# Kernel optimization log

Measured on AMD Instinct MI355X. Metric: run time of the kernel, lower is better.

## Reference

```python
import jax, jax.numpy as jnp
import numpy as np

FEA, DK, H = 512, 64, 8
B, L = 4, 2048
EPS = 1e-5


def _layernorm(x, g, b):
    mu = jnp.mean(x, axis=-1, keepdims=True)
    var = jnp.mean(jnp.square(x - mu), axis=-1, keepdims=True)
    return (x - mu) * jax.lax.rsqrt(var + EPS) * g + b


def setup_inputs() -> dict:
    key = jax.random.key(0)
    ks = jax.random.split(key, 12)
    d = {
        'qx': jax.random.normal(ks[0], (B, L, FEA), jnp.float32),
        'kx': jax.random.normal(ks[1], (B, L, FEA), jnp.float32),
        'vx': jax.random.normal(ks[2], (B, L, FEA), jnp.float32),
        'maskPAD': jax.random.randint(ks[3], (B, L, L), 0, 2, jnp.int32),
        # attention projections (stored as [in, out]); biases zero-init as in module
        'wq': jax.random.normal(ks[4], (FEA, DK * H), jnp.float32) * 0.02,
        'bq': jnp.zeros((DK * H,), jnp.float32),
        'wk': jax.random.normal(ks[5], (FEA, DK * H), jnp.float32) * 0.02,
        'bk': jnp.zeros((DK * H,), jnp.float32),
        'wv': jax.random.normal(ks[6], (FEA, DK * H), jnp.float32) * 0.02,
        'bv': jnp.zeros((DK * H,), jnp.float32),
        'wo': jax.random.normal(ks[7], (DK * H, FEA), jnp.float32) * 0.02,
        'bo': jnp.zeros((FEA,), jnp.float32),
        # FFN
        'w1': jax.random.normal(ks[8], (FEA, 4 * FEA), jnp.float32) * 0.02,
        'b1': jnp.zeros((4 * FEA,), jnp.float32),
        'w2': jax.random.normal(ks[9], (4 * FEA, FEA), jnp.float32) * 0.02,
        'b2': jnp.zeros((FEA,), jnp.float32),
        # layer norms
        'ln1_g': jnp.ones((FEA,), jnp.float32),
        'ln1_b': jnp.zeros((FEA,), jnp.float32),
        'ln2_g': jnp.ones((FEA,), jnp.float32),
        'ln2_b': jnp.zeros((FEA,), jnp.float32),
    }
    return d


def reference(qx, kx, vx, maskPAD, wq, bq, wk, bk, wv, bv, wo, bo,
              w1, b1, w2, b2, ln1_g, ln1_b, ln2_g, ln2_b):
    b, l, _ = qx.shape
    # project and split heads: [B, H, L, DK]
    q = (qx @ wq + bq).reshape(b, l, H, DK).transpose(0, 2, 1, 3)
    k = (kx @ wk + bk).reshape(b, l, H, DK).transpose(0, 2, 1, 3)
    v = (vx @ wv + bv).reshape(b, l, H, DK).transpose(0, 2, 1, 3)
    scores = jnp.einsum('bhqd,bhkd->bhqk', q, k) / np.sqrt(DK)  # [B,H,L,L]
    mask = (maskPAD == 0)[:, None, :, :]
    scores = jnp.where(mask, jnp.float32(-2 ** 15 + 1), scores)
    alpha = jax.nn.softmax(scores, axis=-1)
    z = jnp.einsum('bhqk,bhkd->bhqd', alpha, v)  # [B,H,L,DK]
    z = z.transpose(0, 2, 1, 3).reshape(b, l, H * DK)
    z = z @ wo + bo
    # post-LN FFN block (dropout = identity at inference)
    zn = _layernorm(vx + z, ln1_g, ln1_b)
    ffn = jax.nn.gelu(zn @ w1 + b1, approximate=False) @ w2 + b2
    return _layernorm(zn + ffn, ln2_g, ln2_b)
```

## Files before the change

kernel.cpp:

```cpp
#include <hip/hip_runtime.h>
#include <cstdint>


typedef __bf16 bf16;
typedef __bf16 bf16x4 __attribute__((ext_vector_type(4)));
typedef __bf16 bf16x8 __attribute__((ext_vector_type(8)));
typedef float floatx4 __attribute__((ext_vector_type(4)));

__device__ __forceinline__ floatx4 mfma_bf16(bf16x8 a, bf16x8 b, floatx4 c) {
  return __builtin_amdgcn_mfma_f32_16x16x32_bf16(a, b, c, 0, 0, 0);
}

__device__ __forceinline__ void load_lds_16(const void* g, void* l) {
  auto gp = reinterpret_cast<const void __attribute__((address_space(1)))*>(
      reinterpret_cast<uintptr_t>(g));
  auto lp = reinterpret_cast<void __attribute__((address_space(3)))*>(
      (unsigned int)reinterpret_cast<uintptr_t>(l));
  __builtin_amdgcn_global_load_lds(gp, lp, 16, 0, 0);
}

__device__ __forceinline__ float gelu_f(float x) {
  float t = 0.7978845608f * (x + 0.044715f * x * x * x);
  float e = __builtin_amdgcn_exp2f(t * 2.885390082f);
  float th = 1.0f - 2.0f * __builtin_amdgcn_rcpf(e + 1.0f);
  return 0.5f * x * (1.0f + th);
}

#define PLANE128 2064
#define PLANE64 1040
#define PSTR 72

__global__ void __launch_bounds__(256) transpose4_k(const float* __restrict__ w0,
                                                    const float* __restrict__ w1,
                                                    const float* __restrict__ w2,
                                                    const float* __restrict__ w3,
                                                    bf16* __restrict__ o0,
                                                    bf16* __restrict__ o1,
                                                    bf16* __restrict__ o2,
                                                    bf16* __restrict__ o3) {
  const float* in = (blockIdx.z == 0) ? w0 : (blockIdx.z == 1) ? w1
                    : (blockIdx.z == 2) ? w2 : w3;
  bf16* out = (blockIdx.z == 0) ? o0 : (blockIdx.z == 1) ? o1
              : (blockIdx.z == 2) ? o2 : o3;
  __shared__ float tile[32][33];
  int m0 = blockIdx.x * 32, k0 = blockIdx.y * 32;
  int tx = threadIdx.x, ty = threadIdx.y;
  for (int i = ty; i < 32; i += 8)
    tile[i][tx] = in[(size_t)(k0 + i) * 512 + m0 + tx];
  __syncthreads();
  for (int i = ty; i < 32; i += 8)
    out[(size_t)(m0 + i) * 512 + k0 + tx] = (bf16)tile[tx][i];
}

__global__ void __launch_bounds__(256) transpose_k(const float* __restrict__ in,
                                                   bf16* __restrict__ out,
                                                   int K, int M) {
  __shared__ float tile[32][33];
  int m0 = blockIdx.x * 32, k0 = blockIdx.y * 32;
  int tx = threadIdx.x, ty = threadIdx.y;
  for (int i = ty; i < 32; i += 8)
    tile[i][tx] = in[(size_t)(k0 + i) * M + m0 + tx];
  __syncthreads();
  for (int i = ty; i < 32; i += 8)
    out[(size_t)(m0 + i) * K + k0 + tx] = (bf16)tile[tx][i];
}

__global__ void __launch_bounds__(256) cvt3_k(const float* __restrict__ a,
                                              const float* __restrict__ b,
                                              const float* __restrict__ c,
                                              bf16* __restrict__ out) {
  int seg = blockIdx.x >> 12;
  const float* in = (seg == 0) ? a : (seg == 1) ? b : c;
  int i = ((blockIdx.x & 4095) * 256 + threadIdx.x) * 4;
  float4 v = *(const float4*)(in + i);
  bf16x4 o;
  o[0] = (bf16)v.x; o[1] = (bf16)v.y; o[2] = (bf16)v.z; o[3] = (bf16)v.w;
  *(bf16x4*)(out + (size_t)seg * 4194304 + i) = o;
}

__global__ void __launch_bounds__(256) maskbits_k(const int* __restrict__ m,
                                                  unsigned long long* __restrict__ out) {
  int w = blockIdx.x * 4 + (threadIdx.x >> 6);
  int lane = threadIdx.x & 63;
  int v = m[(size_t)w * 64 + lane];
  unsigned long long b = __ballot(v != 0);
  if (lane == 0) out[w] = b;
}

template <int EPI>
__device__ __forceinline__ void epi_store(void* Cout, int n, int m, int M,
                                          float val) {
  if constexpr (EPI == 1) {
    int bb = n >> 11, l = n & 2047, hh = m >> 6, d = m & 63;
    ((bf16*)Cout)[((size_t)((bb * 8 + hh) * 2048 + l)) * 64 + d] = (bf16)val;
  } else if constexpr (EPI == 2) {
    int bb = n >> 11, l = n & 2047, hh = m >> 6, d = m & 63;
    ((bf16*)Cout)[((size_t)((bb * 8 + hh) * 64 + d)) * 2048 + l] = (bf16)val;
  } else if constexpr (EPI == 3) {
    ((bf16*)Cout)[(size_t)n * M + m] = (bf16)gelu_f(val);
  } else if constexpr (EPI == 4) {
    ((float*)Cout)[(size_t)n * M + m] = val;
  } else {
    ((float*)Cout)[(size_t)n * M + m] += val;
  }
}

template <int EPI, bool TALL>
__global__ void __launch_bounds__(256) gemm_bt(const bf16* __restrict__ A,
                                               const bf16* __restrict__ Bt,
                                               const float* __restrict__ bias,
                                               void* __restrict__ Cout,
                                               int M, int K, int lda, int ldb) {
  __shared__ __attribute__((aligned(16))) char As[8 * PLANE128];
  __shared__ __attribute__((aligned(16))) char Bs[TALL ? 8 * PLANE64 : 8 * PLANE128];
  int tid = threadIdx.x, wave = tid >> 6, lane = tid & 63;
  int lrow = lane & 15, quad = lane >> 4;
  int n0 = blockIdx.y * 128;
  int m0 = blockIdx.x * (TALL ? 64 : 128);
  int wr = wave >> 1, wc = wave & 1;
  floatx4 zero4 = {0.f, 0.f, 0.f, 0.f};
  constexpr int NI = TALL ? 2 : 4;
  floatx4 acc[NI][4];
#pragma unroll
  for (int i = 0; i < NI; ++i)
#pragma unroll
    for (int j = 0; j < 4; ++j) acc[i][j] = zero4;
  for (int k0 = 0; k0 < K; k0 += 64) {
    __syncthreads();
#pragma unroll
    for (int h = 0; h < 2; ++h) {
      int p = wave + 4 * h;
#pragma unroll
      for (int j = 0; j < 2; ++j) {
        int row = j * 64 + lane;
        load_lds_16(A + (size_t)(n0 + row) * lda + k0 + p * 8,
                    As + p * PLANE128 + j * 1024 + lane * 16);
      }
      if constexpr (TALL) {
        load_lds_16(Bt + (size_t)(m0 + lane) * ldb + k0 + p * 8,
                    Bs + p * PLANE64 + lane * 16);
      } else {
#pragma unroll
        for (int j = 0; j < 2; ++j) {
          int row = j * 64 + lane;
          load_lds_16(Bt + (size_t)(m0 + row) * ldb + k0 + p * 8,
                      Bs + p * PLANE128 + j * 1024 + lane * 16);
        }
      }
    }
    __syncthreads();
#pragma unroll
    for (int h = 0; h < 2; ++h) {
      int pb = h * 4 + quad;
      bf16x8 af[NI], bfr[4];
#pragma unroll
      for (int i = 0; i < NI; ++i) {
        int row = (TALL ? wave * 32 : wr * 64) + i * 16 + lrow;
        af[i] = *(const bf16x8*)(As + pb * PLANE128 + row * 16);
      }
#pragma unroll
      for (int j = 0; j < 4; ++j) {
        if constexpr (TALL)
          bfr[j] = *(const bf16x8*)(Bs + pb * PLANE64 + (j * 16 + lrow) * 16);
        else
          bfr[j] = *(const bf16x8*)(Bs + pb * PLANE128 +
                                    (wc * 64 + j * 16 + lrow) * 16);
      }
#pragma unroll
      for (int i = 0; i < NI; ++i)
#pragma unroll
        for (int j = 0; j < 4; ++j)
          acc[i][j] = mfma_bf16(af[i], bfr[j], acc[i][j]);
    }
  }
  float bv[4];
#pragma unroll
  for (int j = 0; j < 4; ++j) {
    int m = m0 + (TALL ? 0 : wc * 64) + j * 16 + lrow;
    bv[j] = (EPI == 5) ? 0.f : bias[m];
  }
#pragma unroll
  for (int i = 0; i < NI; ++i)
#pragma unroll
    for (int j = 0; j < 4; ++j)
#pragma unroll
      for (int r = 0; r < 4; ++r) {
        int n = n0 + (TALL ? wave * 32 : wr * 64) + i * 16 + quad * 4 + r;
        int m = m0 + (TALL ? 0 : wc * 64) + j * 16 + lrow;
        epi_store<EPI>(Cout, n, m, M, acc[i][j][r] + bv[j]);
      }
}

__global__ void __launch_bounds__(256) qkv2_k(const bf16* __restrict__ xall,
                                              const bf16* __restrict__ wqT,
                                              const bf16* __restrict__ wkT,
                                              const bf16* __restrict__ wvT,
                                              const float* __restrict__ bq,
                                              const float* __restrict__ bk,
                                              const float* __restrict__ bv_,
                                              bf16* __restrict__ qh,
                                              bf16* __restrict__ kh,
                                              bf16* __restrict__ vt) {
  __shared__ __attribute__((aligned(16))) char As[8 * PLANE128];
  __shared__ __attribute__((aligned(16))) char Bs[8 * PLANE128];
  int tid = threadIdx.x, wave = tid >> 6, lane = tid & 63;
  int lrow = lane & 15, quad = lane >> 4;
  int seg = blockIdx.y >> 6;
  int n0 = (blockIdx.y & 63) * 128, m0 = blockIdx.x * 128;
  const bf16* A = xall + (size_t)seg * 4194304;
  const bf16* Bt = (seg == 0) ? wqT : (seg == 1) ? wkT : wvT;
  const float* bias = (seg == 0) ? bq : (seg == 1) ? bk : bv_;
  bf16* out = (seg == 0) ? qh : (seg == 1) ? kh : vt;
  int wr = wave >> 1, wc = wave & 1;
  floatx4 zero4 = {0.f, 0.f, 0.f, 0.f};
  floatx4 acc[4][4];
#pragma unroll
  for (int i = 0; i < 4; ++i)
#pragma unroll
    for (int j = 0; j < 4; ++j) acc[i][j] = zero4;
  for (int k0 = 0; k0 < 512; k0 += 64) {
    __syncthreads();
#pragma unroll
    for (int h = 0; h < 2; ++h) {
      int p = wave + 4 * h;
#pragma unroll
      for (int j = 0; j < 2; ++j) {
        int row = j * 64 + lane;
        load_lds_16(A + (size_t)(n0 + row) * 512 + k0 + p * 8,
                    As + p * PLANE128 + j * 1024 + lane * 16);
        load_lds_16(Bt + (size_t)(m0 + row) * 512 + k0 + p * 8,
                    Bs + p * PLANE128 + j * 1024 + lane * 16);
      }
    }
    __syncthreads();
#pragma unroll
    for (int h = 0; h < 2; ++h) {
      int pb = h * 4 + quad;
      bf16x8 af[4], bfr[4];
#pragma unroll
      for (int t = 0; t < 4; ++t) {
        af[t] = *(const bf16x8*)(As + pb * PLANE128 + (wr * 64 + t * 16 + lrow) * 16);
        bfr[t] = *(const bf16x8*)(Bs + pb * PLANE128 + (wc * 64 + t * 16 + lrow) * 16);
      }
#pragma unroll
      for (int i = 0; i < 4; ++i)
#pragma unroll
        for (int j = 0; j < 4; ++j) acc[i][j] = mfma_bf16(af[i], bfr[j], acc[i][j]);
    }
  }
  float bvv[4];
#pragma unroll
  for (int j = 0; j < 4; ++j) bvv[j] = bias[m0 + wc * 64 + j * 16 + lrow];
#pragma unroll
  for (int i = 0; i < 4; ++i)
#pragma unroll
    for (int j = 0; j < 4; ++j)
#pragma unroll
      for (int r = 0; r < 4; ++r) {
        int n = n0 + wr * 64 + i * 16 + quad * 4 + r;
        int m = m0 + wc * 64 + j * 16 + lrow;
        float val = acc[i][j][r] + bvv[j];
        int bb = n >> 11, l = n & 2047, hh = m >> 6, d = m & 63;
        if (seg == 2)
          out[((size_t)((bb * 8 + hh) * 64 + d)) * 2048 + l] = (bf16)val;
        else
          out[((size_t)((bb * 8 + hh) * 2048 + l)) * 64 + d] = (bf16)val;
      }
}

__global__ void __launch_bounds__(256) qkv_k(const float* __restrict__ qx,
                                             const float* __restrict__ kx,
                                             const float* __restrict__ vx,
                                             const bf16* __restrict__ wqT,
                                             const bf16* __restrict__ wkT,
                                             const bf16* __restrict__ wvT,
                                             const float* __restrict__ bq,
                                             const float* __restrict__ bk,
                                             const float* __restrict__ bv_,
                                             bf16* __restrict__ qh,
                                             bf16* __restrict__ kh,
                                             bf16* __restrict__ vt) {
  __shared__ __attribute__((aligned(16))) char As[8 * PLANE128];
  __shared__ __attribute__((aligned(16))) char Bs[8 * PLANE128];
  int tid = threadIdx.x, wave = tid >> 6, lane = tid & 63;
  int lrow = lane & 15, quad = lane >> 4;
  int seg = blockIdx.y >> 6;
  int n0 = (blockIdx.y & 63) * 128, m0 = blockIdx.x * 128;
  const float* Af = (seg == 0) ? qx : (seg == 1) ? kx : vx;
  const bf16* Bt = (seg == 0) ? wqT : (seg == 1) ? wkT : wvT;
  const float* bias = (seg == 0) ? bq : (seg == 1) ? bk : bv_;
  bf16* out = (seg == 0) ? qh : (seg == 1) ? kh : vt;
  int wr = wave >> 1, wc = wave & 1;
  floatx4 zero4 = {0.f, 0.f, 0.f, 0.f};
  floatx4 acc[4][4];
#pragma unroll
  for (int i = 0; i < 4; ++i)
#pragma unroll
    for (int j = 0; j < 4; ++j) acc[i][j] = zero4;
  int arow = tid >> 2, ap = tid & 3;
  for (int k0 = 0; k0 < 512; k0 += 64) {
    bf16x8 a[4];
#pragma unroll
    for (int u = 0; u < 4; ++u) {
      int row = arow + (u & 1) * 64, p = ap + (u >> 1) * 4;
      const float* src = Af + (size_t)(n0 + row) * 512 + k0 + p * 8;
      float4 x0 = *(const float4*)src;
      float4 x1 = *(const float4*)(src + 4);
      a[u][0] = (bf16)x0.x; a[u][1] = (bf16)x0.y; a[u][2] = (bf16)x0.z;
      a[u][3] = (bf16)x0.w; a[u][4] = (bf16)x1.x; a[u][5] = (bf16)x1.y;
      a[u][6] = (bf16)x1.z; a[u][7] = (bf16)x1.w;
    }
    __syncthreads();
#pragma unroll
    for (int u = 0; u < 4; ++u) {
      int row = arow + (u & 1) * 64, p = ap + (u >> 1) * 4;
      *(bf16x8*)(As + p * PLANE128 + row * 16) = a[u];
    }
#pragma unroll
    for (int h = 0; h < 2; ++h) {
      int p = wave + 4 * h;
#pragma unroll
      for (int j = 0; j < 2; ++j) {
        int row = j * 64 + lane;
        load_lds_16(Bt + (size_t)(m0 + row) * 512 + k0 + p * 8,
                    Bs + p * PLANE128 + j * 1024 + lane * 16);
      }
    }
    __syncthreads();
#pragma unroll
    for (int h = 0; h < 2; ++h) {
      int pb = h * 4 + quad;
      bf16x8 af[4], bfr[4];
#pragma unroll
      for (int t = 0; t < 4; ++t) {
        af[t] = *(const bf16x8*)(As + pb * PLANE128 + (wr * 64 + t * 16 + lrow) * 16);
        bfr[t] = *(const bf16x8*)(Bs + pb * PLANE128 + (wc * 64 + t * 16 + lrow) * 16);
      }
#pragma unroll
      for (int i = 0; i < 4; ++i)
#pragma unroll
        for (int j = 0; j < 4; ++j) acc[i][j] = mfma_bf16(af[i], bfr[j], acc[i][j]);
    }
  }
  float bvv[4];
#pragma unroll
  for (int j = 0; j < 4; ++j) bvv[j] = bias[m0 + wc * 64 + j * 16 + lrow];
#pragma unroll
  for (int i = 0; i < 4; ++i)
#pragma unroll
    for (int j = 0; j < 4; ++j)
#pragma unroll
      for (int r = 0; r < 4; ++r) {
        int n = n0 + wr * 64 + i * 16 + quad * 4 + r;
        int m = m0 + wc * 64 + j * 16 + lrow;
        float val = acc[i][j][r] + bvv[j];
        int bb = n >> 11, l = n & 2047, hh = m >> 6, d = m & 63;
        if (seg == 2)
          out[((size_t)((bb * 8 + hh) * 64 + d)) * 2048 + l] = (bf16)val;
        else
          out[((size_t)((bb * 8 + hh) * 2048 + l)) * 64 + d] = (bf16)val;
      }
}

__global__ void __launch_bounds__(256) attn_k(const bf16* __restrict__ Qh,
                                              const bf16* __restrict__ Kh,
                                              const bf16* __restrict__ Vt,
                                              const unsigned long long* __restrict__ MB,
                                              bf16* __restrict__ Z) {
  __shared__ __attribute__((aligned(16))) char Ks[8 * PLANE64];
  __shared__ __attribute__((aligned(16))) char Vs[8 * PLANE64];
  __shared__ __attribute__((aligned(16))) bf16 Pt[4][16 * PSTR];
  int qt = blockIdx.x, h = blockIdx.y, b = blockIdx.z;
  int tid = threadIdx.x, wave = tid >> 6, lane = tid & 63;
  int lrow = lane & 15, quad = lane >> 4;
  int q0 = qt * 64;
  size_t headbase = (size_t)(b * 8 + h) * 2048 * 64;

  const bf16* Qp = Qh + headbase + (size_t)(q0 + wave * 16 + lrow) * 64 + quad * 8;
  bf16x8 qf0 = *(const bf16x8*)Qp;
  bf16x8 qf1 = *(const bf16x8*)(Qp + 32);

  floatx4 zero4 = {0.f, 0.f, 0.f, 0.f};
  floatx4 o_acc[4], acc_l = zero4;
#pragma unroll
  for (int dt = 0; dt < 4; ++dt) o_acc[dt] = zero4;
  bf16x8 ones;
#pragma unroll
  for (int j = 0; j < 8; ++j) ones[j] = (bf16)1.0f;

  const bf16* Vg = Vt + headbase;
  const unsigned long long* MBrow =
      MB + ((size_t)b * 2048 + q0 + wave * 16 + lrow) * 32;
  bf16* Pw = Pt[wave];
  const float C = 0.1803368801f;

  for (int kt = 0; kt < 32; ++kt) {
    int kk0 = kt * 64;
    const bf16* Kg = Kh + headbase + (size_t)kk0 * 64;
    __syncthreads();
#pragma unroll
    for (int j = 0; j < 2; ++j) {
      int p = wave * 2 + j;
      load_lds_16(Kg + (size_t)lane * 64 + p * 8, Ks + p * PLANE64 + lane * 16);
      load_lds_16(Vg + (size_t)lane * 2048 + kk0 + p * 8,
                  Vs + p * PLANE64 + lane * 16);
    }
    unsigned long long mw = MBrow[kt];
    unsigned sx = (unsigned)(mw >> (quad * 4));
    unsigned sy = (unsigned)(mw >> (32 + quad * 4));
    __syncthreads();

#pragma unroll
    for (int nt = 0; nt < 4; ++nt) {
      int R = nt * 16 + lrow;
      bf16x8 k0f = *(const bf16x8*)(Ks + quad * PLANE64 + R * 16);
      bf16x8 k1f = *(const bf16x8*)(Ks + (quad + 4) * PLANE64 + R * 16);
      floatx4 aa = zero4;
      aa = mfma_bf16(k0f, qf0, aa);
      aa = mfma_bf16(k1f, qf1, aa);
      unsigned sel = (nt < 2 ? sx : sy) >> ((nt & 1) * 16);
      bf16x4 pv;
#pragma unroll
      for (int r = 0; r < 4; ++r) {
        float e = __builtin_amdgcn_exp2f(aa[r] * C);
        pv[r] = (bf16)(((sel >> r) & 1u) ? e : 0.f);
      }
      *(bf16x4*)(Pw + lrow * PSTR + nt * 16 + quad * 4) = pv;
    }
    bf16x8 pf0 = *(const bf16x8*)(Pw + lrow * PSTR + quad * 8);
    bf16x8 pf1 = *(const bf16x8*)(Pw + lrow * PSTR + 32 + quad * 8);
    acc_l = mfma_bf16(ones, pf0, acc_l);
    acc_l = mfma_bf16(ones, pf1, acc_l);
#pragma unroll
    for (int dt = 0; dt < 4; ++dt) {
      int R = dt * 16 + lrow;
      bf16x8 v0 = *(const bf16x8*)(Vs + quad * PLANE64 + R * 16);
      bf16x8 v1 = *(const bf16x8*)(Vs + (quad + 4) * PLANE64 + R * 16);
      o_acc[dt] = mfma_bf16(v0, pf0, o_acc[dt]);
      o_acc[dt] = mfma_bf16(v1, pf1, o_acc[dt]);
    }
  }
  float lr = __builtin_amdgcn_rcpf(acc_l[0]);
  size_t zrow = ((size_t)(b * 2048 + q0 + wave * 16 + lrow)) * 512 + h * 64;
#pragma unroll
  for (int dt = 0; dt < 4; ++dt) {
    bf16x4 ov;
#pragma unroll
    for (int r = 0; r < 4; ++r) ov[r] = (bf16)(o_acc[dt][r] * lr);
    *(bf16x4*)(Z + zrow + dt * 16 + quad * 4) = ov;
  }
}

template <bool A_BF16, bool OUT_BF16>
__global__ void __launch_bounds__(256) ln_k(const void* __restrict__ a_,
                                            const float* __restrict__ s,
                                            const float* __restrict__ g,
                                            const float* __restrict__ bta,
                                            void* __restrict__ out_) {
  int row = blockIdx.x * 4 + (threadIdx.x >> 6);
  int lane = threadIdx.x & 63;
  size_t base = (size_t)row * 512 + lane * 8;
  float x[8];
  float4 sa = *(const float4*)(s + base);
  float4 sb = *(const float4*)(s + base + 4);
  if constexpr (A_BF16) {
    bf16x8 av = *(const bf16x8*)((const bf16*)a_ + base);
    x[0] = (float)av[0] + sa.x; x[1] = (float)av[1] + sa.y;
    x[2] = (float)av[2] + sa.z; x[3] = (float)av[3] + sa.w;
    x[4] = (float)av[4] + sb.x; x[5] = (float)av[5] + sb.y;
    x[6] = (float)av[6] + sb.z; x[7] = (float)av[7] + sb.w;
  } else {
    float4 a0 = *(const float4*)((const float*)a_ + base);
    float4 a1 = *(const float4*)((const float*)a_ + base + 4);
    x[0] = a0.x + sa.x; x[1] = a0.y + sa.y; x[2] = a0.z + sa.z; x[3] = a0.w + sa.w;
    x[4] = a1.x + sb.x; x[5] = a1.y + sb.y; x[6] = a1.z + sb.z; x[7] = a1.w + sb.w;
  }
  float sum = 0.f;
#pragma unroll
  for (int i = 0; i < 8; ++i) sum += x[i];
#pragma unroll
  for (int off = 1; off < 64; off <<= 1) sum += __shfl_xor(sum, off, 64);
  float mu = sum * (1.0f / 512.0f);
  float vs = 0.f;
#pragma unroll
  for (int i = 0; i < 8; ++i) { float d = x[i] - mu; vs += d * d; }
#pragma unroll
  for (int off = 1; off < 64; off <<= 1) vs += __shfl_xor(vs, off, 64);
  float rstd = rsqrtf(vs * (1.0f / 512.0f) + 1e-5f);
  float4 g0 = *(const float4*)(g + lane * 8);
  float4 g1 = *(const float4*)(g + lane * 8 + 4);
  float4 b0 = *(const float4*)(bta + lane * 8);
  float4 b1 = *(const float4*)(bta + lane * 8 + 4);
  float gg[8] = {g0.x, g0.y, g0.z, g0.w, g1.x, g1.y, g1.z, g1.w};
  float bb[8] = {b0.x, b0.y, b0.z, b0.w, b1.x, b1.y, b1.z, b1.w};
  if constexpr (OUT_BF16) {
    bf16x8 o;
#pragma unroll
    for (int i = 0; i < 8; ++i)
      o[i] = (bf16)((x[i] - mu) * rstd * gg[i] + bb[i]);
    *(bf16x8*)((bf16*)out_ + base) = o;
  } else {
    float4 o0, o1;
    o0.x = (x[0] - mu) * rstd * gg[0] + bb[0];
    o0.y = (x[1] - mu) * rstd * gg[1] + bb[1];
    o0.z = (x[2] - mu) * rstd * gg[2] + bb[2];
    o0.w = (x[3] - mu) * rstd * gg[3] + bb[3];
    o1.x = (x[4] - mu) * rstd * gg[4] + bb[4];
    o1.y = (x[5] - mu) * rstd * gg[5] + bb[5];
    o1.z = (x[6] - mu) * rstd * gg[6] + bb[6];
    o1.w = (x[7] - mu) * rstd * gg[7] + bb[7];
    *(float4*)((float*)out_ + base) = o0;
    *(float4*)((float*)out_ + base + 4) = o1;
  }
}

extern "C" void kernel_launch(void* const* d_in, const int* in_sizes, int n_in,
                              void* d_out, int out_size, void* d_ws, size_t ws_size,
                              hipStream_t stream) {
  const float* qx = (const float*)d_in[0];
  const float* kx = (const float*)d_in[1];
  const float* vx = (const float*)d_in[2];
  const int* maskPAD = (const int*)d_in[3];
  const float* wq = (const float*)d_in[4];
  const float* bq = (const float*)d_in[5];
  const float* wk = (const float*)d_in[6];
  const float* bk = (const float*)d_in[7];
  const float* wv = (const float*)d_in[8];
  const float* bv = (const float*)d_in[9];
  const float* wo = (const float*)d_in[10];
  const float* bo = (const float*)d_in[11];
  const float* w1 = (const float*)d_in[12];
  const float* b1 = (const float*)d_in[13];
  const float* w2 = (const float*)d_in[14];
  const float* b2 = (const float*)d_in[15];
  const float* g1 = (const float*)d_in[16];
  const float* be1 = (const float*)d_in[17];
  const float* g2 = (const float*)d_in[18];
  const float* be2 = (const float*)d_in[19];

  char* w = (char*)d_ws;
  size_t off = 0;
  auto alloc = [&](size_t bytes) {
    void* p = w + off;
    off += (bytes + 255) & ~(size_t)255;
    return p;
  };
  bf16* wqT = (bf16*)alloc(512 * 512 * 2);
  bf16* wkT = (bf16*)alloc(512 * 512 * 2);
  bf16* wvT = (bf16*)alloc(512 * 512 * 2);
  bf16* woT = (bf16*)alloc(512 * 512 * 2);
  bf16* w1T = (bf16*)alloc(2048 * 512 * 2);
  bf16* w2T = (bf16*)alloc(512 * 2048 * 2);
  unsigned long long* mbits = (unsigned long long*)alloc((size_t)4 * 2048 * 32 * 8);
  size_t xall_bytes = (size_t)3 * 8192 * 512 * 2;
  size_t act4 = (size_t)8192 * 512 * 2;
  bool fast = (off + xall_bytes + 4 * (act4 + 256)) <= ws_size;
  bf16* xall = fast ? (bf16*)alloc(xall_bytes) : nullptr;
  bf16* qh = (bf16*)alloc(act4);
  bf16* kh = (bf16*)alloc(act4);
  bf16* vt = (bf16*)alloc(act4);
  bf16* z = (bf16*)alloc(act4);
  float* s12;
  bf16* zn;
  if (fast) {
    s12 = (float*)xall;
    zn = (bf16*)((char*)xall + (size_t)8192 * 512 * 4);
  } else {
    s12 = (float*)qh;
    zn = vt;
  }
  size_t h1_bytes = (size_t)8192 * 2048 * 2;
  bool big = (off + h1_bytes) <= ws_size;
  bf16* h1 = big ? (bf16*)alloc(h1_bytes) : z;

  dim3 tb(32, 8);
  transpose4_k<<<dim3(16, 16, 4), tb, 0, stream>>>(wq, wk, wv, wo, wqT, wkT, wvT, woT);
  transpose_k<<<dim3(64, 16), tb, 0, stream>>>(w1, w1T, 512, 2048);
  transpose_k<<<dim3(16, 64), tb, 0, stream>>>(w2, w2T, 2048, 512);
  maskbits_k<<<65536, 256, 0, stream>>>(maskPAD, mbits);
  if (fast) {
    cvt3_k<<<12288, 256, 0, stream>>>(qx, kx, vx, xall);
    qkv2_k<<<dim3(4, 192), 256, 0, stream>>>(xall, wqT, wkT, wvT, bq, bk, bv,
                                             qh, kh, vt);
  } else {
    qkv_k<<<dim3(4, 192), 256, 0, stream>>>(qx, kx, vx, wqT, wkT, wvT, bq, bk,
                                            bv, qh, kh, vt);
  }
  attn_k<<<dim3(32, 8, 4), 256, 0, stream>>>(qh, kh, vt, mbits, z);
  gemm_bt<4, true><<<dim3(8, 64), 256, 0, stream>>>(z, woT, bo, s12, 512, 512,
                                                    512, 512);
  ln_k<false, true><<<2048, 256, 0, stream>>>(vx, s12, g1, be1, zn);
  if (big) {
    gemm_bt<3, false><<<dim3(16, 64), 256, 0, stream>>>(zn, w1T, b1, h1, 2048,
                                                        512, 512, 512);
    gemm_bt<4, true><<<dim3(8, 64), 256, 0, stream>>>(h1, w2T, b2, s12, 512,
                                                      2048, 2048, 2048);
  } else {
    for (int p = 0; p < 4; ++p) {
      gemm_bt<3, true><<<dim3(8, 64), 256, 0, stream>>>(
          zn, w1T + (size_t)p * 512 * 512, b1 + p * 512, h1, 512, 512, 512, 512);
      if (p == 0)
        gemm_bt<4, true><<<dim3(8, 64), 256, 0, stream>>>(
            h1, w2T + p * 512, b2, s12, 512, 512, 512, 2048);
      else
        gemm_bt<5, true><<<dim3(8, 64), 256, 0, stream>>>(
            h1, w2T + p * 512, nullptr, s12, 512, 512, 512, 2048);
    }
  }
  ln_k<true, false><<<2048, 256, 0, stream>>>(zn, s12, g2, be2, (float*)d_out);
}
```

Baseline: 469.1 us.

## Double-buffer LDS tiles in GEMM, QKV and attention kernels to overlap loads

```diff
diff --git a/kernel.cpp b/kernel.cpp
--- a/kernel.cpp
+++ b/kernel.cpp
@@ -90,13 +90,7 @@
 template <int EPI>
 __device__ __forceinline__ void epi_store(void* Cout, int n, int m, int M,
                                           float val) {
-  if constexpr (EPI == 1) {
-    int bb = n >> 11, l = n & 2047, hh = m >> 6, d = m & 63;
-    ((bf16*)Cout)[((size_t)((bb * 8 + hh) * 2048 + l)) * 64 + d] = (bf16)val;
-  } else if constexpr (EPI == 2) {
-    int bb = n >> 11, l = n & 2047, hh = m >> 6, d = m & 63;
-    ((bf16*)Cout)[((size_t)((bb * 8 + hh) * 64 + d)) * 2048 + l] = (bf16)val;
-  } else if constexpr (EPI == 3) {
+  if constexpr (EPI == 3) {
     ((bf16*)Cout)[(size_t)n * M + m] = (bf16)gelu_f(val);
   } else if constexpr (EPI == 4) {
     ((float*)Cout)[(size_t)n * M + m] = val;
@@ -111,8 +105,11 @@
                                                const float* __restrict__ bias,
                                                void* __restrict__ Cout,
                                                int M, int K, int lda, int ldb) {
-  __shared__ __attribute__((aligned(16))) char As[8 * PLANE128];
-  __shared__ __attribute__((aligned(16))) char Bs[TALL ? 8 * PLANE64 : 8 * PLANE128];
+  constexpr int BK = TALL ? 64 : 32;
+  constexpr int NPL = BK / 8;
+  constexpr int BSZ = TALL ? NPL * PLANE64 : NPL * PLANE128;
+  __shared__ __attribute__((aligned(16))) char As[2][NPL * PLANE128];
+  __shared__ __attribute__((aligned(16))) char Bs[2][BSZ];
   int tid = threadIdx.x, wave = tid >> 6, lane = tid & 63;
   int lrow = lane & 15, quad = lane >> 4;
   int n0 = blockIdx.y * 128;
@@ -125,49 +122,68 @@
   for (int i = 0; i < NI; ++i)
 #pragma unroll
     for (int j = 0; j < 4; ++j) acc[i][j] = zero4;
-  for (int k0 = 0; k0 < K; k0 += 64) {
-    __syncthreads();
-#pragma unroll
-    for (int h = 0; h < 2; ++h) {
-      int p = wave + 4 * h;
+
+  auto stage = [&](int buf, int k0) {
+    if constexpr (TALL) {
+#pragma unroll
+      for (int h = 0; h < 2; ++h) {
+        int p = wave + 4 * h;
+#pragma unroll
+        for (int j = 0; j < 2; ++j) {
+          int row = j * 64 + lane;
+          load_lds_16(A + (size_t)(n0 + row) * lda + k0 + p * 8,
+                      As[buf] + p * PLANE128 + j * 1024 + lane * 16);
+        }
+        load_lds_16(Bt + (size_t)(m0 + lane) * ldb + k0 + p * 8,
+                    Bs[buf] + p * PLANE64 + lane * 16);
+      }
+    } else {
 #pragma unroll
       for (int j = 0; j < 2; ++j) {
         int row = j * 64 + lane;
-        load_lds_16(A + (size_t)(n0 + row) * lda + k0 + p * 8,
-                    As + p * PLANE128 + j * 1024 + lane * 16);
-      }
-      if constexpr (TALL) {
-        load_lds_16(Bt + (size_t)(m0 + lane) * ldb + k0 + p * 8,
-                    Bs + p * PLANE64 + lane * 16);
-      } else {
-#pragma unroll
-        for (int j = 0; j < 2; ++j) {
-          int row = j * 64 + lane;
-          load_lds_16(Bt + (size_t)(m0 + row) * ldb + k0 + p * 8,
-                      Bs + p * PLANE128 + j * 1024 + lane * 16);
-        }
-      }
-    }
+        load_lds_16(A + (size_t)(n0 + row) * lda + k0 + wave * 8,
+                    As[buf] + wave * PLANE128 + j * 1024 + lane * 16);
+        load_lds_16(Bt + (size_t)(m0 + row) * ldb + k0 + wave * 8,
+                    Bs[buf] + wave * PLANE128 + j * 1024 + lane * 16);
+      }
+    }
+  };
+
+  stage(0, 0);
+  int nit = K / BK;
+  for (int it = 0; it < nit; ++it) {
+    int cur = it & 1;
     __syncthreads();
-#pragma unroll
-    for (int h = 0; h < 2; ++h) {
-      int pb = h * 4 + quad;
-      bf16x8 af[NI], bfr[4];
-#pragma unroll
-      for (int i = 0; i < NI; ++i) {
-        int row = (TALL ? wave * 32 : wr * 64) + i * 16 + lrow;
-        af[i] = *(const bf16x8*)(As + pb * PLANE128 + row * 16);
-      }
-#pragma unroll
-      for (int j = 0; j < 4; ++j) {
-        if constexpr (TALL)
-          bfr[j] = *(const bf16x8*)(Bs + pb * PLANE64 + (j * 16 + lrow) * 16);
-        else
-          bfr[j] = *(const bf16x8*)(Bs + pb * PLANE128 +
-                                    (wc * 64 + j * 16 + lrow) * 16);
-      }
-#pragma unroll
-      for (int i = 0; i < NI; ++i)
+    if (it + 1 < nit) stage(cur ^ 1, (it + 1) * BK);
+    if constexpr (TALL) {
+#pragma unroll
+      for (int h = 0; h < 2; ++h) {
+        int pb = h * 4 + quad;
+        bf16x8 af[2], bfr[4];
+#pragma unroll
+        for (int i = 0; i < 2; ++i)
+          af[i] = *(const bf16x8*)(As[cur] + pb * PLANE128 +
+                                   (wave * 32 + i * 16 + lrow) * 16);
+#pragma unroll
+        for (int j = 0; j < 4; ++j)
+          bfr[j] = *(const bf16x8*)(Bs[cur] + pb * PLANE64 + (j * 16 + lrow) * 16);
+#pragma unroll
+        for (int i = 0; i < 2; ++i)
+#pragma unroll
+          for (int j = 0; j < 4; ++j)
+            acc[i][j] = mfma_bf16(af[i], bfr[j], acc[i][j]);
+      }
+    } else {
+      bf16x8 af[4], bfr[4];
+#pragma unroll
+      for (int t = 0; t < 4; ++t) {
+        af[t] = *(const bf16x8*)(As[cur] + quad * PLANE128 +
+                                 (wr * 64 + t * 16 + lrow) * 16);
+        bfr[t] = *(const bf16x8*)(Bs[cur] + quad * PLANE128 +
+                                  (wc * 64 + t * 16 + lrow) * 16);
+      }
+#pragma unroll
+      for (int i = 0; i < 4; ++i)
 #pragma unroll
         for (int j = 0; j < 4; ++j)
           acc[i][j] = mfma_bf16(af[i], bfr[j], acc[i][j]);
@@ -201,8 +217,8 @@
                                               bf16* __restrict__ qh,
                                               bf16* __restrict__ kh,
                                               bf16* __restrict__ vt) {
-  __shared__ __attribute__((aligned(16))) char As[8 * PLANE128];
-  __shared__ __attribute__((aligned(16))) char Bs[8 * PLANE128];
+  __shared__ __attribute__((aligned(16))) char As[2][4 * PLANE128];
+  __shared__ __attribute__((aligned(16))) char Bs[2][4 * PLANE128];
   int tid = threadIdx.x, wave = tid >> 6, lane = tid & 63;
   int lrow = lane & 15, quad = lane >> 4;
   int seg = blockIdx.y >> 6;
@@ -218,35 +234,35 @@
   for (int i = 0; i < 4; ++i)
 #pragma unroll
     for (int j = 0; j < 4; ++j) acc[i][j] = zero4;
-  for (int k0 = 0; k0 < 512; k0 += 64) {
+
+  auto stage = [&](int buf, int k0) {
+#pragma unroll
+    for (int j = 0; j < 2; ++j) {
+      int row = j * 64 + lane;
+      load_lds_16(A + (size_t)(n0 + row) * 512 + k0 + wave * 8,
+                  As[buf] + wave * PLANE128 + j * 1024 + lane * 16);
+      load_lds_16(Bt + (size_t)(m0 + row) * 512 + k0 + wave * 8,
+                  Bs[buf] + wave * PLANE128 + j * 1024 + lane * 16);
+    }
+  };
+
+  stage(0, 0);
+  for (int it = 0; it < 16; ++it) {
+    int cur = it & 1;
     __syncthreads();
-#pragma unroll
-    for (int h = 0; h < 2; ++h) {
-      int p = wave + 4 * h;
-#pragma unroll
-      for (int j = 0; j < 2; ++j) {
-        int row = j * 64 + lane;
-        load_lds_16(A + (size_t)(n0 + row) * 512 + k0 + p * 8,
-                    As + p * PLANE128 + j * 1024 + lane * 16);
-        load_lds_16(Bt + (size_t)(m0 + row) * 512 + k0 + p * 8,
-                    Bs + p * PLANE128 + j * 1024 + lane * 16);
-      }
-    }
-    __syncthreads();
-#pragma unroll
-    for (int h = 0; h < 2; ++h) {
-      int pb = h * 4 + quad;
-      bf16x8 af[4], bfr[4];
-#pragma unroll
-      for (int t = 0; t < 4; ++t) {
-        af[t] = *(const bf16x8*)(As + pb * PLANE128 + (wr * 64 + t * 16 + lrow) * 16);
-        bfr[t] = *(const bf16x8*)(Bs + pb * PLANE128 + (wc * 64 + t * 16 + lrow) * 16);
-      }
-#pragma unroll
-      for (int i = 0; i < 4; ++i)
-#pragma unroll
-        for (int j = 0; j < 4; ++j) acc[i][j] = mfma_bf16(af[i], bfr[j], acc[i][j]);
-    }
+    if (it + 1 < 16) stage(cur ^ 1, (it + 1) * 32);
+    bf16x8 af[4], bfr[4];
+#pragma unroll
+    for (int t = 0; t < 4; ++t) {
+      af[t] = *(const bf16x8*)(As[cur] + quad * PLANE128 +
+                               (wr * 64 + t * 16 + lrow) * 16);
+      bfr[t] = *(const bf16x8*)(Bs[cur] + quad * PLANE128 +
+                                (wc * 64 + t * 16 + lrow) * 16);
+    }
+#pragma unroll
+    for (int i = 0; i < 4; ++i)
+#pragma unroll
+      for (int j = 0; j < 4; ++j) acc[i][j] = mfma_bf16(af[i], bfr[j], acc[i][j]);
   }
   float bvv[4];
 #pragma unroll
@@ -254,18 +270,22 @@
 #pragma unroll
   for (int i = 0; i < 4; ++i)
 #pragma unroll
-    for (int j = 0; j < 4; ++j)
-#pragma unroll
-      for (int r = 0; r < 4; ++r) {
-        int n = n0 + wr * 64 + i * 16 + quad * 4 + r;
-        int m = m0 + wc * 64 + j * 16 + lrow;
-        float val = acc[i][j][r] + bvv[j];
-        int bb = n >> 11, l = n & 2047, hh = m >> 6, d = m & 63;
-        if (seg == 2)
-          out[((size_t)((bb * 8 + hh) * 64 + d)) * 2048 + l] = (bf16)val;
-        else
-          out[((size_t)((bb * 8 + hh) * 2048 + l)) * 64 + d] = (bf16)val;
-      }
+    for (int j = 0; j < 4; ++j) {
+      int n_ = n0 + wr * 64 + i * 16 + quad * 4;
+      int m_ = m0 + wc * 64 + j * 16 + lrow;
+      int bb = n_ >> 11, l = n_ & 2047, hh = m_ >> 6, d = m_ & 63;
+      if (seg == 2) {
+        bf16x4 ov;
+#pragma unroll
+        for (int r = 0; r < 4; ++r) ov[r] = (bf16)(acc[i][j][r] + bvv[j]);
+        *(bf16x4*)(out + ((size_t)((bb * 8 + hh) * 64 + d)) * 2048 + l) = ov;
+      } else {
+#pragma unroll
+        for (int r = 0; r < 4; ++r)
+          out[((size_t)((bb * 8 + hh) * 2048 + l + r)) * 64 + d] =
+              (bf16)(acc[i][j][r] + bvv[j]);
+      }
+    }
 }
 
 __global__ void __launch_bounds__(256) qkv_k(const float* __restrict__ qx,
@@ -367,8 +387,8 @@
                                               const bf16* __restrict__ Vt,
                                               const unsigned long long* __restrict__ MB,
                                               bf16* __restrict__ Z) {
-  __shared__ __attribute__((aligned(16))) char Ks[8 * PLANE64];
-  __shared__ __attribute__((aligned(16))) char Vs[8 * PLANE64];
+  __shared__ __attribute__((aligned(16))) char Ks[2][8 * PLANE64];
+  __shared__ __attribute__((aligned(16))) char Vs[2][8 * PLANE64];
   __shared__ __attribute__((aligned(16))) bf16 Pt[4][16 * PSTR];
   int qt = blockIdx.x, h = blockIdx.y, b = blockIdx.z;
   int tid = threadIdx.x, wave = tid >> 6, lane = tid & 63;
@@ -394,27 +414,33 @@
   bf16* Pw = Pt[wave];
   const float C = 0.1803368801f;
 
-  for (int kt = 0; kt < 32; ++kt) {
+  auto stage_kv = [&](int buf, int kt) {
     int kk0 = kt * 64;
     const bf16* Kg = Kh + headbase + (size_t)kk0 * 64;
-    __syncthreads();
 #pragma unroll
     for (int j = 0; j < 2; ++j) {
       int p = wave * 2 + j;
-      load_lds_16(Kg + (size_t)lane * 64 + p * 8, Ks + p * PLANE64 + lane * 16);
+      load_lds_16(Kg + (size_t)lane * 64 + p * 8,
+                  Ks[buf] + p * PLANE64 + lane * 16);
       load_lds_16(Vg + (size_t)lane * 2048 + kk0 + p * 8,
-                  Vs + p * PLANE64 + lane * 16);
-    }
+                  Vs[buf] + p * PLANE64 + lane * 16);
+    }
+  };
+
+  stage_kv(0, 0);
+  for (int kt = 0; kt < 32; ++kt) {
+    int cur = kt & 1;
+    __syncthreads();
+    if (kt + 1 < 32) stage_kv(cur ^ 1, kt + 1);
     unsigned long long mw = MBrow[kt];
     unsigned sx = (unsigned)(mw >> (quad * 4));
     unsigned sy = (unsigned)(mw >> (32 + quad * 4));
-    __syncthreads();
 
 #pragma unroll
     for (int nt = 0; nt < 4; ++nt) {
       int R = nt * 16 + lrow;
-      bf16x8 k0f = *(const bf16x8*)(Ks + quad * PLANE64 + R * 16);
-      bf16x8 k1f = *(const bf16x8*)(Ks + (quad + 4) * PLANE64 + R * 16);
+      bf16x8 k0f = *(const bf16x8*)(Ks[cur] + quad * PLANE64 + R * 16);
+      bf16x8 k1f = *(const bf16x8*)(Ks[cur] + (quad + 4) * PLANE64 + R * 16);
       floatx4 aa = zero4;
       aa = mfma_bf16(k0f, qf0, aa);
       aa = mfma_bf16(k1f, qf1, aa);
@@ -434,8 +460,8 @@
 #pragma unroll
     for (int dt = 0; dt < 4; ++dt) {
       int R = dt * 16 + lrow;
-      bf16x8 v0 = *(const bf16x8*)(Vs + quad * PLANE64 + R * 16);
-      bf16x8 v1 = *(const bf16x8*)(Vs + (quad + 4) * PLANE64 + R * 16);
+      bf16x8 v0 = *(const bf16x8*)(Vs[cur] + quad * PLANE64 + R * 16);
+      bf16x8 v1 = *(const bf16x8*)(Vs[cur] + (quad + 4) * PLANE64 + R * 16);
       o_acc[dt] = mfma_bf16(v0, pf0, o_acc[dt]);
       o_acc[dt] = mfma_bf16(v1, pf1, o_acc[dt]);
     }
```

Result: no change. 470.0 us (+0.2%).
